# Performance work log

Hardware: AMD Instinct MI355X
Metric: run time of the kernel (lower is better)

Reference implementation:

```python
import jax, jax.numpy as jnp
import numpy as np

N_USERS = 100_000
N_ENTITIES = 200_000
N_EDGES = 1_000_000
NNZ = 1_000_000
C = 64          # embedding dim
N_FACTORS = 4
N_REL_M1 = 10   # n_relations - 1
N_HOPS = 2
TEMP = 0.2


def setup_inputs() -> dict:
    key = jax.random.key(0)
    ks = jax.random.split(key, 10)
    return {
        'user_emb': jax.random.normal(ks[0], (N_USERS, C), jnp.float32) * 0.1,
        'entity_emb': jax.random.normal(ks[1], (N_ENTITIES, C), jnp.float32) * 0.1,
        'latent_emb': jax.random.normal(ks[2], (N_FACTORS, C), jnp.float32) * 0.1,
        'weight': jax.random.normal(ks[3], (N_REL_M1, C), jnp.float32) * 0.1,
        'disen_weight_att': jax.random.normal(ks[4], (N_FACTORS, N_REL_M1), jnp.float32) * 0.1,
        'edge_index': jax.random.randint(ks[5], (2, N_EDGES), 0, N_ENTITIES, dtype=jnp.int32),
        'edge_type': jax.random.randint(ks[6], (N_EDGES,), 1, N_REL_M1 + 1, dtype=jnp.int32),
        'inter_rows': jax.random.randint(ks[7], (NNZ,), 0, N_USERS, dtype=jnp.int32),
        'inter_cols': jax.random.randint(ks[8], (NNZ,), 0, N_ENTITIES, dtype=jnp.int32),
        'inter_vals': jax.random.uniform(ks[9], (NNZ,), jnp.float32),
    }


def _l2norm(x):
    # F.normalize(x, dim=1) with eps=1e-12
    n = jnp.linalg.norm(x, axis=1, keepdims=True)
    return x / jnp.maximum(n, 1e-12)


def _mutual_information(disen_weight_att):
    disen_T = disen_weight_att.T                                    # [R-1, F]
    nd = disen_T / jnp.linalg.norm(disen_T, axis=1, keepdims=True)
    pos_scores = jnp.sum(nd * nd, axis=1)
    ttl_scores = jnp.sum(disen_T @ disen_weight_att, axis=1)
    pos = jnp.exp(pos_scores / TEMP)
    ttl = jnp.exp(ttl_scores / TEMP)
    return -jnp.sum(jnp.log(pos / ttl))


def reference(user_emb, entity_emb, latent_emb, weight, disen_weight_att,
              edge_index, edge_type, inter_rows, inter_cols, inter_vals):
    entity_res = entity_emb
    user_res = user_emb
    cor = _mutual_information(disen_weight_att)

    head, tail = edge_index[0], edge_index[1]
    # edge degree for scatter_mean (constant across hops)
    cnt = jax.ops.segment_sum(jnp.ones((N_EDGES,), jnp.float32), head,
                              num_segments=N_ENTITIES)
    inv_cnt = 1.0 / jnp.maximum(cnt, 1.0)

    for _ in range(N_HOPS):
        # KG aggregate: gather tail entities, modulate by relation, scatter-mean to head
        rel = weight[edge_type - 1]                                  # [E, C]
        neigh = entity_emb[tail] * rel                               # [E, C]
        entity_agg = jax.ops.segment_sum(neigh, head, num_segments=N_ENTITIES)
        entity_agg = entity_agg * inv_cnt[:, None]

        # user -> latent factor attention
        score = jax.nn.softmax(user_emb @ latent_emb.T, axis=1)[:, :, None]  # [U, F, 1]

        # sparse user aggregate: interact_mat @ entity_emb
        user_agg = jax.ops.segment_sum(inter_vals[:, None] * entity_emb[inter_cols],
                                       inter_rows, num_segments=N_USERS)     # [U, C]

        disen_weight = jax.nn.softmax(disen_weight_att, axis=-1) @ weight    # [F, C]
        user_agg = user_agg * jnp.sum(disen_weight[None] * score, axis=1) + user_agg

        entity_emb = _l2norm(entity_agg)
        user_emb = _l2norm(user_agg)
        entity_res = entity_res + entity_emb
        user_res = user_res + user_emb

    return entity_res, user_res, cor
```

## Files before the change

kernel.cpp:

```cpp
#include <hip/hip_runtime.h>
#include <math.h>

#define N_USERS    100000
#define N_ENTITIES 200000
#define N_EDGES    1000000
#define NNZ        1000000
#define CDIM       64
#define N_FACTORS  4
#define N_REL      10
#define TEMP       0.2f

#define CB         1024
#define NBE        196
#define NBU        98
#define ACHUNK     4096
#define GA         245
#define GCVT       6250
#define KG_BLOCKS  6250
#define USER_BLOCKS 3125
#define PCHUNK     4096
#define GPE        49
#define GPU_       25

typedef unsigned int u32;
typedef unsigned short u16;
typedef unsigned char u8;

#if defined(__has_builtin)
#if __has_builtin(__builtin_amdgcn_cvt_pk_f32_fp8) && __has_builtin(__builtin_amdgcn_cvt_pk_fp8_f32)
#define HAVE_HW_FP8 1
#endif
#endif

__device__ __forceinline__ float bflo(u32 w) { return __uint_as_float(w << 16); }
__device__ __forceinline__ float bfhi(u32 w) { return __uint_as_float(w & 0xFFFF0000u); }
__device__ __forceinline__ u16 f2bf(float f) {
    u32 u = __float_as_uint(f);
    u32 r = u + 0x7FFFu + ((u >> 16) & 1u);
    return (u16)(r >> 16);
}
__device__ __forceinline__ void unpack8_bf(uint4 rv, float* x) {
    x[0] = bflo(rv.x); x[1] = bfhi(rv.x);
    x[2] = bflo(rv.y); x[3] = bfhi(rv.y);
    x[4] = bflo(rv.z); x[5] = bfhi(rv.z);
    x[6] = bflo(rv.w); x[7] = bfhi(rv.w);
}
__device__ __forceinline__ uint4 pack8_bf(const float* x) {
    uint4 o;
    o.x = (u32)f2bf(x[0]) | ((u32)f2bf(x[1]) << 16);
    o.y = (u32)f2bf(x[2]) | ((u32)f2bf(x[3]) << 16);
    o.z = (u32)f2bf(x[4]) | ((u32)f2bf(x[5]) << 16);
    o.w = (u32)f2bf(x[6]) | ((u32)f2bf(x[7]) << 16);
    return o;
}

#ifndef HAVE_HW_FP8
__device__ __forceinline__ float fp8_dec1(u32 b) {
    u32 s = b >> 7, em = b & 0x7F;
    float mag;
    if (em < 8) mag = (float)em * 0.001953125f;
    else {
        u32 bits = (((em >> 3) + 120u) << 23) | ((em & 7u) << 20);
        mag = __uint_as_float(bits);
    }
    return s ? -mag : mag;
}
__device__ __forceinline__ u32 fp8_enc1(float f) {
    float a = fabsf(f);
    u32 s = (__float_as_uint(f) >> 31) << 7;
    if (a < 0.015625f) {
        int n = (int)rintf(a * 512.0f);
        return s | (u32)n;
    }
    u32 u = __float_as_uint(a);
    u32 r = u + 0x0007FFFFu + ((u >> 20) & 1u);
    int ee = (int)((r >> 23) & 0xFF) - 127 + 7;
    if (ee >= 16) return s | 0x7Eu;
    return s | ((u32)ee << 3) | ((r >> 20) & 7u);
}
#endif

__device__ __forceinline__ void unpack8_fp8(uint2 rv, float* x) {
#ifdef HAVE_HW_FP8
    typedef float floatx2 __attribute__((ext_vector_type(2)));
    floatx2 a0 = __builtin_amdgcn_cvt_pk_f32_fp8(rv.x, false);
    floatx2 a1 = __builtin_amdgcn_cvt_pk_f32_fp8(rv.x, true);
    floatx2 a2 = __builtin_amdgcn_cvt_pk_f32_fp8(rv.y, false);
    floatx2 a3 = __builtin_amdgcn_cvt_pk_f32_fp8(rv.y, true);
    x[0] = a0.x; x[1] = a0.y; x[2] = a1.x; x[3] = a1.y;
    x[4] = a2.x; x[5] = a2.y; x[6] = a3.x; x[7] = a3.y;
#else
    x[0] = fp8_dec1(rv.x & 0xFF);         x[1] = fp8_dec1((rv.x >> 8) & 0xFF);
    x[2] = fp8_dec1((rv.x >> 16) & 0xFF); x[3] = fp8_dec1(rv.x >> 24);
    x[4] = fp8_dec1(rv.y & 0xFF);         x[5] = fp8_dec1((rv.y >> 8) & 0xFF);
    x[6] = fp8_dec1((rv.y >> 16) & 0xFF); x[7] = fp8_dec1(rv.y >> 24);
#endif
}
__device__ __forceinline__ uint2 pack8_fp8(const float* x) {
    uint2 o;
#ifdef HAVE_HW_FP8
    int v0 = 0, v1 = 0;
    v0 = __builtin_amdgcn_cvt_pk_fp8_f32(x[0], x[1], v0, false);
    v0 = __builtin_amdgcn_cvt_pk_fp8_f32(x[2], x[3], v0, true);
    v1 = __builtin_amdgcn_cvt_pk_fp8_f32(x[4], x[5], v1, false);
    v1 = __builtin_amdgcn_cvt_pk_fp8_f32(x[6], x[7], v1, true);
    o.x = (u32)v0; o.y = (u32)v1;
#else
    o.x = fp8_enc1(x[0]) | (fp8_enc1(x[1]) << 8) | (fp8_enc1(x[2]) << 16) | (fp8_enc1(x[3]) << 24);
    o.y = fp8_enc1(x[4]) | (fp8_enc1(x[5]) << 8) | (fp8_enc1(x[6]) << 16) | (fp8_enc1(x[7]) << 24);
#endif
    return o;
}

__device__ __forceinline__ void fma_rowW(float* acc, uint2 rv, int rel,
                                         const float* __restrict__ weight, int seg) {
    float x[8]; unpack8_fp8(rv, x);
    const float4* wp = (const float4*)(weight + rel * CDIM + seg * 8);
    float4 w0 = wp[0], w1 = wp[1];
    acc[0] += x[0] * w0.x; acc[1] += x[1] * w0.y;
    acc[2] += x[2] * w0.z; acc[3] += x[3] * w0.w;
    acc[4] += x[4] * w1.x; acc[5] += x[5] * w1.y;
    acc[6] += x[6] * w1.z; acc[7] += x[7] * w1.w;
}
__device__ __forceinline__ void fma_rowV(float* acc, uint2 rv, float v) {
    float x[8]; unpack8_fp8(rv, x);
    #pragma unroll
    for (int k = 0; k < 8; ++k) acc[k] += v * x[k];
}

__device__ void dev_cvt(int b, const float* __restrict__ in, u8* __restrict__ out) {
    int i = b * 256 + threadIdx.x;
    const float4* p = (const float4*)(in + (size_t)i * 8);
    float4 a = p[0], bb = p[1];
    float x[8] = {a.x, a.y, a.z, a.w, bb.x, bb.y, bb.z, bb.w};
    *(uint2*)(out + (size_t)i * 8) = pack8_fp8(x);
}

__device__ void dev_coarse_hist(int b, const int* __restrict__ idx, int n,
                                int* __restrict__ bhist) {
    __shared__ int lh[256];
    int t = threadIdx.x;
    lh[t] = 0; __syncthreads();
    int base = b * ACHUNK;
    #pragma unroll
    for (int k = 0; k < 16; ++k) {
        int i = base + k * 256 + t;
        if (i < n) atomicAdd(&lh[idx[i] >> 10], 1);
    }
    __syncthreads();
    if (lh[t]) atomicAdd(&bhist[t], lh[t]);
}

__device__ void dev_disen_cor(const float* __restrict__ att,
                              const float* __restrict__ weight,
                              float* __restrict__ dw, float* __restrict__ cor_out) {
    int tid = threadIdx.x;
    int f = tid >> 6, c = tid & 63;
    float m = -1e30f;
    for (int r = 0; r < N_REL; ++r) m = fmaxf(m, att[f * N_REL + r]);
    float e[N_REL], s = 0.0f;
    for (int r = 0; r < N_REL; ++r) { e[r] = __expf(att[f * N_REL + r] - m); s += e[r]; }
    float acc = 0.0f;
    for (int r = 0; r < N_REL; ++r) acc += (e[r] / s) * weight[r * CDIM + c];
    dw[f * CDIM + c] = acc;

    if (tid == 0) {
        float rowsum[N_FACTORS];
        for (int ff = 0; ff < N_FACTORS; ++ff) {
            float ss = 0.0f;
            for (int j = 0; j < N_REL; ++j) ss += att[ff * N_REL + j];
            rowsum[ff] = ss;
        }
        float cor = 0.0f;
        for (int i = 0; i < N_REL; ++i) {
            float nsq = 0.0f, ttl = 0.0f;
            for (int ff = 0; ff < N_FACTORS; ++ff) {
                float a = att[ff * N_REL + i];
                nsq += a * a;
                ttl += a * rowsum[ff];
            }
            float n = sqrtf(nsq);
            float pos = 0.0f;
            for (int ff = 0; ff < N_FACTORS; ++ff) {
                float a = att[ff * N_REL + i] / n;
                pos += a * a;
            }
            cor += (ttl - pos) / TEMP;
        }
        *cor_out = cor;
    }
}

__global__ __launch_bounds__(256) void prep_kernel(const float* __restrict__ entity_emb,
                                                   u8* __restrict__ ef8,
                                                   const int* __restrict__ head,
                                                   const int* __restrict__ inter_rows,
                                                   int* __restrict__ bhe,
                                                   int* __restrict__ bhu,
                                                   const float* __restrict__ att,
                                                   const float* __restrict__ weight,
                                                   float* __restrict__ dw,
                                                   float* __restrict__ cor_out) {
    int bid = blockIdx.x;
    if (bid < GCVT)                 dev_cvt(bid, entity_emb, ef8);
    else if (bid < GCVT + GA)       dev_coarse_hist(bid - GCVT, head, N_EDGES, bhe);
    else if (bid < GCVT + 2 * GA)   dev_coarse_hist(bid - GCVT - GA, inter_rows, NNZ, bhu);
    else                            dev_disen_cor(att, weight, dw, cor_out);
}

__device__ void dev_bucket_scan(const int* __restrict__ bhist, int nb,
                                int* __restrict__ bbase, int* __restrict__ gcur,
                                int* __restrict__ off_n) {
    __shared__ int s[256];
    int t = threadIdx.x;
    int v = (t < nb) ? bhist[t] : 0;
    s[t] = v; __syncthreads();
    #pragma unroll
    for (int d = 1; d < 256; d <<= 1) {
        int x = (t >= d) ? s[t - d] : 0;
        __syncthreads();
        s[t] += x;
        __syncthreads();
    }
    int excl = s[t] - v;
    if (t < nb) { bbase[t] = excl; gcur[t] = excl; }
    if (t == nb - 1) { bbase[nb] = s[t]; *off_n = s[t]; }
}

__global__ __launch_bounds__(256) void bucket_scan2(const int* __restrict__ bhe,
                                                    const int* __restrict__ bhu,
                                                    int* __restrict__ bbe, int* __restrict__ bbu,
                                                    int* __restrict__ gce, int* __restrict__ gcu,
                                                    int* __restrict__ eoffN, int* __restrict__ uoffN) {
    if (blockIdx.x == 0) dev_bucket_scan(bhe, NBE, bbe, gce, eoffN);
    else                 dev_bucket_scan(bhu, NBU, bbu, gcu, uoffN);
}

__device__ void dev_bin_edges(int b, const int* __restrict__ head,
                              const int* __restrict__ tail, const int* __restrict__ etype,
                              int* __restrict__ gcur, int* __restrict__ binbuf) {
    __shared__ int lh[256], lbase[256];
    int t = threadIdx.x;
    lh[t] = 0; __syncthreads();
    int base = b * ACHUNK;
    int rec[16], rnk[16], bkt[16];
    #pragma unroll
    for (int k = 0; k < 16; ++k) {
        int i = base + k * 256 + t;
        rnk[k] = -1; rec[k] = 0; bkt[k] = 0;
        if (i < N_EDGES) {
            int h = head[i];
            bkt[k] = h >> 10;
            rec[k] = ((h & 1023) << 22) | ((etype[i] - 1) << 18) | tail[i];
            rnk[k] = atomicAdd(&lh[bkt[k]], 1);
        }
    }
    __syncthreads();
    lbase[t] = lh[t] ? atomicAdd(&gcur[t], lh[t]) : 0;
    __syncthreads();
    #pragma unroll
    for (int k = 0; k < 16; ++k)
        if (rnk[k] >= 0) binbuf[lbase[bkt[k]] + rnk[k]] = rec[k];
}

__device__ void dev_bin_inter(int b, const int* __restrict__ rows,
                              const int* __restrict__ cols, const float* __restrict__ vals,
                              int* __restrict__ gcur, int2* __restrict__ binbuf) {
    __shared__ int lh[256], lbase[256];
    int t = threadIdx.x;
    lh[t] = 0; __syncthreads();
    int base = b * ACHUNK;
    int recx[16], recy[16], rnk[16], bkt[16];
    #pragma unroll
    for (int k = 0; k < 16; ++k) {
        int i = base + k * 256 + t;
        rnk[k] = -1; recx[k] = 0; recy[k] = 0; bkt[k] = 0;
        if (i < NNZ) {
            int r = rows[i];
            bkt[k] = r >> 10;
            recx[k] = ((r & 1023) << 18) | cols[i];
            recy[k] = __float_as_int(vals[i]);
            rnk[k] = atomicAdd(&lh[bkt[k]], 1);
        }
    }
    __syncthreads();
    lbase[t] = lh[t] ? atomicAdd(&gcur[t], lh[t]) : 0;
    __syncthreads();
    #pragma unroll
    for (int k = 0; k < 16; ++k)
        if (rnk[k] >= 0) {
            int2 p; p.x = recx[k]; p.y = recy[k];
            binbuf[lbase[bkt[k]] + rnk[k]] = p;
        }
}

__global__ __launch_bounds__(256) void bin_kernel(const int* __restrict__ head,
                                                  const int* __restrict__ tail,
                                                  const int* __restrict__ etype,
                                                  const int* __restrict__ rows,
                                                  const int* __restrict__ cols,
                                                  const float* __restrict__ vals,
                                                  int* __restrict__ gce, int* __restrict__ gcu,
                                                  int* __restrict__ bine, int2* __restrict__ binu) {
    int bid = blockIdx.x;
    if (bid < GA) dev_bin_edges(bid, head, tail, etype, gce, bine);
    else          dev_bin_inter(bid - GA, rows, cols, vals, gcu, binu);
}

__device__ void dev_build_e(int b, const int* __restrict__ bbase,
                            const int* __restrict__ binbuf,
                            int* __restrict__ eoff, int* __restrict__ epk,
                            int* __restrict__ dbinE) {
    __shared__ int lh[CB];
    __shared__ int ss[256];
    __shared__ int ldeg[64];
    int t = threadIdx.x;
    int bstart = bbase[b], bend = bbase[b + 1];
    #pragma unroll
    for (int k = 0; k < 4; ++k) lh[t * 4 + k] = 0;
    if (t < 64) ldeg[t] = 0;
    __syncthreads();
    for (int j = bstart + t; j < bend; j += 256)
        atomicAdd(&lh[(u32)binbuf[j] >> 22], 1);
    __syncthreads();
    int v[4], acc = 0;
    #pragma unroll
    for (int k = 0; k < 4; ++k) { v[k] = lh[t * 4 + k]; acc += v[k]; }
    ss[t] = acc; __syncthreads();
    #pragma unroll
    for (int d = 1; d < 256; d <<= 1) {
        int x = (t >= d) ? ss[t - d] : 0;
        __syncthreads();
        ss[t] += x;
        __syncthreads();
    }
    int excl = ss[t] - acc;
    int hbase = b * CB;
    #pragma unroll
    for (int k = 0; k < 4; ++k) {
        int hl = t * 4 + k;
        int h = hbase + hl;
        if (h < N_ENTITIES) {
            eoff[h] = bstart + excl;
            atomicAdd(&ldeg[63 - min(v[k], 63)], 1);
        }
        lh[hl] = excl;
        excl += v[k];
    }
    __syncthreads();
    if (t < 64 && ldeg[t]) atomicAdd(&dbinE[t], ldeg[t]);
    for (int j = bstart + t; j < bend; j += 256) {
        int rec = binbuf[j];
        int pos = atomicAdd(&lh[(u32)rec >> 22], 1);
        epk[bstart + pos] = rec & 0x3FFFFF;
    }
}

__device__ void dev_build_u(int b, const int* __restrict__ bbase,
                            const int2* __restrict__ binbuf,
                            int* __restrict__ uoff, int2* __restrict__ ucv,
                            int* __restrict__ dbinU) {
    __shared__ int lh[CB];
    __shared__ int ss[256];
    __shared__ int ldeg[64];
    int t = threadIdx.x;
    int bstart = bbase[b], bend = bbase[b + 1];
    #pragma unroll
    for (int k = 0; k < 4; ++k) lh[t * 4 + k] = 0;
    if (t < 64) ldeg[t] = 0;
    __syncthreads();
    for (int j = bstart + t; j < bend; j += 256)
        atomicAdd(&lh[(u32)binbuf[j].x >> 18], 1);
    __syncthreads();
    int v[4], acc = 0;
    #pragma unroll
    for (int k = 0; k < 4; ++k) { v[k] = lh[t * 4 + k]; acc += v[k]; }
    ss[t] = acc; __syncthreads();
    #pragma unroll
    for (int d = 1; d < 256; d <<= 1) {
        int x = (t >= d) ? ss[t - d] : 0;
        __syncthreads();
        ss[t] += x;
        __syncthreads();
    }
    int excl = ss[t] - acc;
    int ubase = b * CB;
    #pragma unroll
    for (int k = 0; k < 4; ++k) {
        int ul = t * 4 + k;
        int u = ubase + ul;
        if (u < N_USERS) {
            uoff[u] = bstart + excl;
            atomicAdd(&ldeg[63 - min(v[k], 63)], 1);
        }
        lh[ul] = excl;
        excl += v[k];
    }
    __syncthreads();
    if (t < 64 && ldeg[t]) atomicAdd(&dbinU[t], ldeg[t]);
    for (int j = bstart + t; j < bend; j += 256) {
        int2 rec = binbuf[j];
        int pos = atomicAdd(&lh[(u32)rec.x >> 18], 1);
        int2 out; out.x = rec.x & 0x3FFFF; out.y = rec.y;
        ucv[bstart + pos] = out;
    }
}

__global__ __launch_bounds__(256) void build_kernel(const int* __restrict__ bbe,
                                                    const int* __restrict__ bbu,
                                                    const int* __restrict__ bine,
                                                    const int2* __restrict__ binu,
                                                    int* __restrict__ eoff, int* __restrict__ epk,
                                                    int* __restrict__ uoff, int2* __restrict__ ucv,
                                                    int* __restrict__ dbinE, int* __restrict__ dbinU) {
    int bid = blockIdx.x;
    if (bid < NBE) dev_build_e(bid, bbe, bine, eoff, epk, dbinE);
    else           dev_build_u(bid - NBE, bbu, binu, uoff, ucv, dbinU);
}

__global__ void deg_scan(const int* __restrict__ dbinE, const int* __restrict__ dbinU,
                         int* __restrict__ curE, int* __restrict__ curU) {
    int t = threadIdx.x;
    if (t == 0) { int run = 0; for (int b = 0; b < 64; ++b) { curE[b] = run; run += dbinE[b]; } }
    if (t == 1) { int run = 0; for (int b = 0; b < 64; ++b) { curU[b] = run; run += dbinU[b]; } }
}

__device__ void dev_perm(int b, int n, const int* __restrict__ off,
                         int* __restrict__ gcur, int2* __restrict__ perm) {
    __shared__ int lh[64], lbase[64];
    int t = threadIdx.x;
    if (t < 64) lh[t] = 0;
    __syncthreads();
    int base = b * PCHUNK;
    int rnk[16], bin[16], deg[16], st[16];
    #pragma unroll
    for (int k = 0; k < 16; ++k) {
        int i = base + k * 256 + t;
        rnk[k] = -1;
        if (i < n) {
            int s0 = off[i], s1 = off[i + 1];
            deg[k] = s1 - s0; st[k] = s0;
            bin[k] = 63 - min(deg[k], 63);
            rnk[k] = atomicAdd(&lh[bin[k]], 1);
        }
    }
    __syncthreads();
    if (t < 64) lbase[t] = lh[t] ? atomicAdd(&gcur[t], lh[t]) : 0;
    __syncthreads();
    #pragma unroll
    for (int k = 0; k < 16; ++k)
        if (rnk[k] >= 0) {
            int i = base + k * 256 + t;
            int2 p;
            p.x = (int)(((u32)min(deg[k], 16383) << 18) | (u32)i);
            p.y = st[k];
            perm[lbase[bin[k]] + rnk[k]] = p;
        }
}

__global__ __launch_bounds__(256) void perm_kernel(const int* __restrict__ eoff,
                                                   const int* __restrict__ uoff,
                                                   int* __restrict__ curE, int* __restrict__ curU,
                                                   int2* __restrict__ permE, int2* __restrict__ permU) {
    int bid = blockIdx.x;
    if (bid < GPE) dev_perm(bid, N_ENTITIES, eoff, curE, permE);
    else           dev_perm(bid - GPE, N_USERS, uoff, curU, permU);
}

__device__ void dev_kg_hop(int widg, const u8* __restrict__ esrc,
                           const int2* __restrict__ permE,
                           const int* __restrict__ epk,
                           const float* __restrict__ weight,
                           const float* __restrict__ emb0,
                           u8* __restrict__ enew, float* __restrict__ eres, int last) {
    int lane = threadIdx.x & 63;
    int slot = lane >> 3, seg = lane & 7;
    int2 pe = permE[widg * 8 + slot];
    u32 px = (u32)pe.x;
    int d = px >> 18, h = (int)(px & 0x3FFFFu), s = pe.y;
    int dmax = d;
    dmax = max(dmax, __shfl_xor(dmax, 8, 64));
    dmax = max(dmax, __shfl_xor(dmax, 16, 64));
    dmax = max(dmax, __shfl_xor(dmax, 32, 64));

    float acc[8];
    #pragma unroll
    for (int k = 0; k < 8; ++k) acc[k] = 0.0f;
    const uint2 uz = make_uint2(0u, 0u);

    for (int it = 0; it < dmax; it += 4) {
        int p0 = (it     < d) ? epk[s + it]     : 0;
        int p1 = (it + 1 < d) ? epk[s + it + 1] : 0;
        int p2 = (it + 2 < d) ? epk[s + it + 2] : 0;
        int p3 = (it + 3 < d) ? epk[s + it + 3] : 0;
        uint2 rv0 = (it     < d) ? *(const uint2*)(esrc + (size_t)(p0 & 0x3FFFF) * CDIM + seg * 8) : uz;
        uint2 rv1 = (it + 1 < d) ? *(const uint2*)(esrc + (size_t)(p1 & 0x3FFFF) * CDIM + seg * 8) : uz;
        uint2 rv2 = (it + 2 < d) ? *(const uint2*)(esrc + (size_t)(p2 & 0x3FFFF) * CDIM + seg * 8) : uz;
        uint2 rv3 = (it + 3 < d) ? *(const uint2*)(esrc + (size_t)(p3 & 0x3FFFF) * CDIM + seg * 8) : uz;
        fma_rowW(acc, rv0, p0 >> 18, weight, seg);
        fma_rowW(acc, rv1, p1 >> 18, weight, seg);
        fma_rowW(acc, rv2, p2 >> 18, weight, seg);
        fma_rowW(acc, rv3, p3 >> 18, weight, seg);
    }
    float inv = 1.0f / fmaxf((float)d, 1.0f);
    float ssq = 0.0f;
    #pragma unroll
    for (int k = 0; k < 8; ++k) { acc[k] *= inv; ssq += acc[k] * acc[k]; }
    ssq += __shfl_xor(ssq, 1, 64);
    ssq += __shfl_xor(ssq, 2, 64);
    ssq += __shfl_xor(ssq, 4, 64);
    float rn = 1.0f / fmaxf(sqrtf(ssq), 1e-12f);
    #pragma unroll
    for (int k = 0; k < 8; ++k) acc[k] *= rn;

    size_t base = (size_t)h * CDIM + seg * 8;
    if (!last) {
        *(uint2*)(enew + base) = pack8_fp8(acc);
    } else {
        uint2 pv = *(const uint2*)(esrc + base);
        float o0[8]; unpack8_fp8(pv, o0);
        float4 a = *(const float4*)(emb0 + base);
        float4 b = *(const float4*)(emb0 + base + 4);
        float4 r0, r1;
        r0.x = a.x + o0[0] + acc[0]; r0.y = a.y + o0[1] + acc[1];
        r0.z = a.z + o0[2] + acc[2]; r0.w = a.w + o0[3] + acc[3];
        r1.x = b.x + o0[4] + acc[4]; r1.y = b.y + o0[5] + acc[5];
        r1.z = b.z + o0[6] + acc[6]; r1.w = b.w + o0[7] + acc[7];
        *(float4*)(eres + base) = r0;
        *(float4*)(eres + base + 4) = r1;
    }
}

__device__ void dev_user_hop(int widg, const float* __restrict__ uoldf,
                             const u16* __restrict__ uoldb,
                             const u8* __restrict__ esrc,
                             const int2* __restrict__ permU,
                             const int2* __restrict__ ucv,
                             const float* __restrict__ latent,
                             const float* __restrict__ dw,
                             const float* __restrict__ uemb0,
                             u16* __restrict__ unew, float* __restrict__ ures, int last) {
    int lane = threadIdx.x & 63;
    int slot = lane >> 3, seg = lane & 7;
    int2 pe = permU[widg * 8 + slot];
    u32 px = (u32)pe.x;
    int d = px >> 18, u = (int)(px & 0x3FFFFu), s = pe.y;
    int dmax = d;
    dmax = max(dmax, __shfl_xor(dmax, 8, 64));
    dmax = max(dmax, __shfl_xor(dmax, 16, 64));
    dmax = max(dmax, __shfl_xor(dmax, 32, 64));

    float acc[8];
    #pragma unroll
    for (int k = 0; k < 8; ++k) acc[k] = 0.0f;
    const uint2 uz = make_uint2(0u, 0u);
    const int2 cz = make_int2(0, 0);

    for (int it = 0; it < dmax; it += 4) {
        int2 c0 = (it     < d) ? ucv[s + it]     : cz;
        int2 c1 = (it + 1 < d) ? ucv[s + it + 1] : cz;
        int2 c2 = (it + 2 < d) ? ucv[s + it + 2] : cz;
        int2 c3 = (it + 3 < d) ? ucv[s + it + 3] : cz;
        uint2 rv0 = (it     < d) ? *(const uint2*)(esrc + (size_t)c0.x * CDIM + seg * 8) : uz;
        uint2 rv1 = (it + 1 < d) ? *(const uint2*)(esrc + (size_t)c1.x * CDIM + seg * 8) : uz;
        uint2 rv2 = (it + 2 < d) ? *(const uint2*)(esrc + (size_t)c2.x * CDIM + seg * 8) : uz;
        uint2 rv3 = (it + 3 < d) ? *(const uint2*)(esrc + (size_t)c3.x * CDIM + seg * 8) : uz;
        fma_rowV(acc, rv0, __int_as_float(c0.y));
        fma_rowV(acc, rv1, __int_as_float(c1.y));
        fma_rowV(acc, rv2, __int_as_float(c2.y));
        fma_rowV(acc, rv3, __int_as_float(c3.y));
    }

    float uo[8];
    size_t ubase = (size_t)u * CDIM + seg * 8;
    if (uoldb) {
        uint4 pv = *(const uint4*)(uoldb + ubase);
        unpack8_bf(pv, uo);
    } else {
        float4 a = *(const float4*)(uoldf + ubase);
        float4 b = *(const float4*)(uoldf + ubase + 4);
        uo[0] = a.x; uo[1] = a.y; uo[2] = a.z; uo[3] = a.w;
        uo[4] = b.x; uo[5] = b.y; uo[6] = b.z; uo[7] = b.w;
    }
    float dts[N_FACTORS];
    #pragma unroll
    for (int f = 0; f < N_FACTORS; ++f) {
        const float4* lp = (const float4*)(latent + f * CDIM + seg * 8);
        float4 l0 = lp[0], l1 = lp[1];
        float p = uo[0] * l0.x + uo[1] * l0.y + uo[2] * l0.z + uo[3] * l0.w +
                  uo[4] * l1.x + uo[5] * l1.y + uo[6] * l1.z + uo[7] * l1.w;
        p += __shfl_xor(p, 1, 64);
        p += __shfl_xor(p, 2, 64);
        p += __shfl_xor(p, 4, 64);
        dts[f] = p;
    }
    float m = fmaxf(fmaxf(dts[0], dts[1]), fmaxf(dts[2], dts[3]));
    float e0 = __expf(dts[0] - m), e1 = __expf(dts[1] - m);
    float e2 = __expf(dts[2] - m), e3 = __expf(dts[3] - m);
    float inv_ssum = 1.0f / (e0 + e1 + e2 + e3);
    e0 *= inv_ssum; e1 *= inv_ssum; e2 *= inv_ssum; e3 *= inv_ssum;

    const float4* d0p = (const float4*)(dw + 0 * CDIM + seg * 8);
    const float4* d1p = (const float4*)(dw + 1 * CDIM + seg * 8);
    const float4* d2p = (const float4*)(dw + 2 * CDIM + seg * 8);
    const float4* d3p = (const float4*)(dw + 3 * CDIM + seg * 8);
    float4 ga0 = d0p[0], ga1 = d0p[1];
    float4 gb0 = d1p[0], gb1 = d1p[1];
    float4 gc0 = d2p[0], gc1 = d2p[1];
    float4 gd0 = d3p[0], gd1 = d3p[1];
    float g[8];
    g[0] = e0 * ga0.x + e1 * gb0.x + e2 * gc0.x + e3 * gd0.x;
    g[1] = e0 * ga0.y + e1 * gb0.y + e2 * gc0.y + e3 * gd0.y;
    g[2] = e0 * ga0.z + e1 * gb0.z + e2 * gc0.z + e3 * gd0.z;
    g[3] = e0 * ga0.w + e1 * gb0.w + e2 * gc0.w + e3 * gd0.w;
    g[4] = e0 * ga1.x + e1 * gb1.x + e2 * gc1.x + e3 * gd1.x;
    g[5] = e0 * ga1.y + e1 * gb1.y + e2 * gc1.y + e3 * gd1.y;
    g[6] = e0 * ga1.z + e1 * gb1.z + e2 * gc1.z + e3 * gd1.z;
    g[7] = e0 * ga1.w + e1 * gb1.w + e2 * gc1.w + e3 * gd1.w;

    float ssq = 0.0f;
    #pragma unroll
    for (int k = 0; k < 8; ++k) {
        acc[k] = acc[k] * (1.0f + g[k]);
        ssq += acc[k] * acc[k];
    }
    ssq += __shfl_xor(ssq, 1, 64);
    ssq += __shfl_xor(ssq, 2, 64);
    ssq += __shfl_xor(ssq, 4, 64);
    float rn = 1.0f / fmaxf(sqrtf(ssq), 1e-12f);
    #pragma unroll
    for (int k = 0; k < 8; ++k) acc[k] *= rn;

    if (!last) {
        *(uint4*)(unew + ubase) = pack8_bf(acc);
    } else {
        float4 a = *(const float4*)(uemb0 + ubase);
        float4 b = *(const float4*)(uemb0 + ubase + 4);
        float4 r0, r1;
        r0.x = a.x + uo[0] + acc[0]; r0.y = a.y + uo[1] + acc[1];
        r0.z = a.z + uo[2] + acc[2]; r0.w = a.w + uo[3] + acc[3];
        r1.x = b.x + uo[4] + acc[4]; r1.y = b.y + uo[5] + acc[5];
        r1.z = b.z + uo[6] + acc[6]; r1.w = b.w + uo[7] + acc[7];
        *(float4*)(ures + ubase) = r0;
        *(float4*)(ures + ubase + 4) = r1;
    }
}

__global__ __launch_bounds__(256) void hop_kernel(const u8* __restrict__ e_src,
                                                  const int2* __restrict__ permE,
                                                  const int* __restrict__ epk,
                                                  const float* __restrict__ weight,
                                                  const float* __restrict__ entity_emb,
                                                  u8* __restrict__ eA,
                                                  float* __restrict__ eres,
                                                  const float* __restrict__ uoldf,
                                                  const u16* __restrict__ uoldb,
                                                  const int2* __restrict__ permU,
                                                  const int2* __restrict__ ucv,
                                                  const float* __restrict__ latent,
                                                  const float* __restrict__ dw,
                                                  const float* __restrict__ user_emb,
                                                  u16* __restrict__ uA,
                                                  float* __restrict__ ures,
                                                  int last) {
    int bid = blockIdx.x;
    int wave = threadIdx.x >> 6;
    if (bid < KG_BLOCKS) {
        dev_kg_hop(bid * 4 + wave, e_src, permE, epk, weight, entity_emb, eA, eres, last);
    } else {
        dev_user_hop((bid - KG_BLOCKS) * 4 + wave, uoldf, uoldb, e_src, permU, ucv,
                     latent, dw, user_emb, uA, ures, last);
    }
}

static inline size_t align16(size_t x) { return (x + 15) & ~(size_t)15; }

extern "C" void kernel_launch(void* const* d_in, const int* in_sizes, int n_in,
                              void* d_out, int out_size, void* d_ws, size_t ws_size,
                              hipStream_t stream) {
    const float* user_emb   = (const float*)d_in[0];
    const float* entity_emb = (const float*)d_in[1];
    const float* latent_emb = (const float*)d_in[2];
    const float* weight     = (const float*)d_in[3];
    const float* att        = (const float*)d_in[4];
    const int*   edge_index = (const int*)d_in[5];
    const int*   edge_type  = (const int*)d_in[6];
    const int*   inter_rows = (const int*)d_in[7];
    const int*   inter_cols = (const int*)d_in[8];
    const float* inter_vals = (const float*)d_in[9];

    float* eres = (float*)d_out;
    float* ures = eres + (size_t)N_ENTITIES * CDIM;
    float* cor  = ures + (size_t)N_USERS * CDIM;

    char* ws = (char*)d_ws;
    u8*    ef8   = (u8*)ws;   ws += align16(sizeof(u8) * (size_t)N_ENTITIES * CDIM);
    u8*    eA    = (u8*)ws;   ws += align16(sizeof(u8) * (size_t)N_ENTITIES * CDIM);
    u16*   uA    = (u16*)ws;  ws += align16(sizeof(u16) * (size_t)N_USERS * CDIM);
    int*   eoff  = (int*)ws;  ws += align16(sizeof(int) * (N_ENTITIES + 1));
    int*   epk   = (int*)ws;  ws += align16(sizeof(int) * N_EDGES);
    int*   uoff  = (int*)ws;  ws += align16(sizeof(int) * (N_USERS + 1));
    int2*  ucv   = (int2*)ws; ws += align16(sizeof(int2) * NNZ);
    int*   bine  = (int*)ws;  ws += align16(sizeof(int) * N_EDGES);
    int2*  binu  = (int2*)ws; ws += align16(sizeof(int2) * NNZ);
    int*   ctrs  = (int*)ws;  ws += align16(sizeof(int) * 640);
    int*   bbe   = (int*)ws;  ws += align16(sizeof(int) * 257);
    int*   bbu   = (int*)ws;  ws += align16(sizeof(int) * 257);
    int*   gce   = (int*)ws;  ws += align16(sizeof(int) * 256);
    int*   gcu   = (int*)ws;  ws += align16(sizeof(int) * 256);
    int*   curE  = (int*)ws;  ws += align16(sizeof(int) * 64);
    int*   curU  = (int*)ws;  ws += align16(sizeof(int) * 64);
    int2*  permE = (int2*)ws; ws += align16(sizeof(int2) * N_ENTITIES);
    int2*  permU = (int2*)ws; ws += align16(sizeof(int2) * N_USERS);
    float* dw    = (float*)ws; ws += align16(sizeof(float) * N_FACTORS * CDIM);

    int* bhe   = ctrs;
    int* bhu   = ctrs + 256;
    int* dbinE = ctrs + 512;
    int* dbinU = ctrs + 576;

    const int* head = edge_index;
    const int* tail = edge_index + N_EDGES;

    (void)hipMemsetAsync(ctrs, 0, sizeof(int) * 640, stream);

    prep_kernel<<<GCVT + 2 * GA + 1, 256, 0, stream>>>(entity_emb, ef8, head, inter_rows,
                                                       bhe, bhu, att, weight, dw, cor);
    bucket_scan2<<<2, 256, 0, stream>>>(bhe, bhu, bbe, bbu, gce, gcu,
                                        eoff + N_ENTITIES, uoff + N_USERS);
    bin_kernel<<<2 * GA, 256, 0, stream>>>(head, tail, edge_type,
                                           inter_rows, inter_cols, inter_vals,
                                           gce, gcu, bine, binu);
    build_kernel<<<NBE + NBU, 256, 0, stream>>>(bbe, bbu, bine, binu,
                                                eoff, epk, uoff, ucv, dbinE, dbinU);
    deg_scan<<<1, 64, 0, stream>>>(dbinE, dbinU, curE, curU);
    perm_kernel<<<GPE + GPU_, 256, 0, stream>>>(eoff, uoff, curE, curU, permE, permU);

    hop_kernel<<<KG_BLOCKS + USER_BLOCKS, 256, 0, stream>>>(
        ef8, permE, epk, weight, entity_emb, eA, eres,
        user_emb, (const u16*)nullptr, permU, ucv, latent_emb, dw, user_emb, uA, ures, 0);
    hop_kernel<<<KG_BLOCKS + USER_BLOCKS, 256, 0, stream>>>(
        eA, permE, epk, weight, entity_emb, (u8*)nullptr, eres,
        (const float*)nullptr, uA, permU, ucv, latent_emb, dw, user_emb, (u16*)nullptr, ures, 1);
}
```

Measured before the change: 216.0 us.

## Fold bucket/degree scans into consumer kernels, interleave hop work, unroll gathers by 8

Removes the separate bucket_scan2 and deg_scan launches. Each bin, build and perm block now recomputes the small prefix scan in LDS and uses zeroed atomic cursors offset by that scan. The hop kernel interleaves user and KG blocks (every third block is a user block) so the two workloads balance across the grid. The gather loops in both the KG and user paths are unrolled from 4 to 8 loads to keep more memory requests in flight. The cost is redundant per-block scan work and higher register pressure in the gather loops.

After: 223.0 us. 3.2% more time.

```diff
diff --git a/kernel.cpp b/kernel.cpp
--- a/kernel.cpp
+++ b/kernel.cpp
@@ -16,8 +16,9 @@
 #define ACHUNK     4096
 #define GA         245
 #define GCVT       6250
-#define KG_BLOCKS  6250
-#define USER_BLOCKS 3125
+#define KG_WAVES   25000
+#define USER_WAVES 12500
+#define HOP_BLOCKS 9375
 #define PCHUNK     4096
 #define GPE        49
 #define GPU_       25
@@ -128,6 +129,22 @@
     for (int k = 0; k < 8; ++k) acc[k] += v * x[k];
 }
 
+__device__ __forceinline__ void lds_scan256(const int* __restrict__ hist, int* sbase,
+                                            int* stmp) {
+    int t = threadIdx.x;
+    int v = hist[t];
+    stmp[t] = v; __syncthreads();
+    #pragma unroll
+    for (int d = 1; d < 256; d <<= 1) {
+        int x = (t >= d) ? stmp[t - d] : 0;
+        __syncthreads();
+        stmp[t] += x;
+        __syncthreads();
+    }
+    sbase[t] = stmp[t] - v;
+    __syncthreads();
+}
+
 __device__ void dev_cvt(int b, const float* __restrict__ in, u8* __restrict__ out) {
     int i = b * 256 + threadIdx.x;
     const float4* p = (const float4*)(in + (size_t)i * 8);
@@ -208,39 +225,14 @@
     else                            dev_disen_cor(att, weight, dw, cor_out);
 }
 
-__device__ void dev_bucket_scan(const int* __restrict__ bhist, int nb,
-                                int* __restrict__ bbase, int* __restrict__ gcur,
-                                int* __restrict__ off_n) {
-    __shared__ int s[256];
-    int t = threadIdx.x;
-    int v = (t < nb) ? bhist[t] : 0;
-    s[t] = v; __syncthreads();
-    #pragma unroll
-    for (int d = 1; d < 256; d <<= 1) {
-        int x = (t >= d) ? s[t - d] : 0;
-        __syncthreads();
-        s[t] += x;
-        __syncthreads();
-    }
-    int excl = s[t] - v;
-    if (t < nb) { bbase[t] = excl; gcur[t] = excl; }
-    if (t == nb - 1) { bbase[nb] = s[t]; *off_n = s[t]; }
-}
-
-__global__ __launch_bounds__(256) void bucket_scan2(const int* __restrict__ bhe,
-                                                    const int* __restrict__ bhu,
-                                                    int* __restrict__ bbe, int* __restrict__ bbu,
-                                                    int* __restrict__ gce, int* __restrict__ gcu,
-                                                    int* __restrict__ eoffN, int* __restrict__ uoffN) {
-    if (blockIdx.x == 0) dev_bucket_scan(bhe, NBE, bbe, gce, eoffN);
-    else                 dev_bucket_scan(bhu, NBU, bbu, gcu, uoffN);
-}
-
 __device__ void dev_bin_edges(int b, const int* __restrict__ head,
                               const int* __restrict__ tail, const int* __restrict__ etype,
-                              int* __restrict__ gcur, int* __restrict__ binbuf) {
+                              const int* __restrict__ bhist,
+                              int* __restrict__ zcur, int* __restrict__ binbuf) {
+    __shared__ int sbase[256], stmp[256];
     __shared__ int lh[256], lbase[256];
     int t = threadIdx.x;
+    lds_scan256(bhist, sbase, stmp);
     lh[t] = 0; __syncthreads();
     int base = b * ACHUNK;
     int rec[16], rnk[16], bkt[16];
@@ -256,7 +248,7 @@
         }
     }
     __syncthreads();
-    lbase[t] = lh[t] ? atomicAdd(&gcur[t], lh[t]) : 0;
+    lbase[t] = lh[t] ? (sbase[t] + atomicAdd(&zcur[t], lh[t])) : 0;
     __syncthreads();
     #pragma unroll
     for (int k = 0; k < 16; ++k)
@@ -265,9 +257,12 @@
 
 __device__ void dev_bin_inter(int b, const int* __restrict__ rows,
                               const int* __restrict__ cols, const float* __restrict__ vals,
-                              int* __restrict__ gcur, int2* __restrict__ binbuf) {
+                              const int* __restrict__ bhist,
+                              int* __restrict__ zcur, int2* __restrict__ binbuf) {
+    __shared__ int sbase[256], stmp[256];
     __shared__ int lh[256], lbase[256];
     int t = threadIdx.x;
+    lds_scan256(bhist, sbase, stmp);
     lh[t] = 0; __syncthreads();
     int base = b * ACHUNK;
     int recx[16], recy[16], rnk[16], bkt[16];
@@ -284,7 +279,7 @@
         }
     }
     __syncthreads();
-    lbase[t] = lh[t] ? atomicAdd(&gcur[t], lh[t]) : 0;
+    lbase[t] = lh[t] ? (sbase[t] + atomicAdd(&zcur[t], lh[t])) : 0;
     __syncthreads();
     #pragma unroll
     for (int k = 0; k < 16; ++k)
@@ -300,22 +295,26 @@
                                                   const int* __restrict__ rows,
                                                   const int* __restrict__ cols,
                                                   const float* __restrict__ vals,
-                                                  int* __restrict__ gce, int* __restrict__ gcu,
+                                                  const int* __restrict__ bhe,
+                                                  const int* __restrict__ bhu,
+                                                  int* __restrict__ zce, int* __restrict__ zcu,
                                                   int* __restrict__ bine, int2* __restrict__ binu) {
     int bid = blockIdx.x;
-    if (bid < GA) dev_bin_edges(bid, head, tail, etype, gce, bine);
-    else          dev_bin_inter(bid - GA, rows, cols, vals, gcu, binu);
-}
-
-__device__ void dev_build_e(int b, const int* __restrict__ bbase,
+    if (bid < GA) dev_bin_edges(bid, head, tail, etype, bhe, zce, bine);
+    else          dev_bin_inter(bid - GA, rows, cols, vals, bhu, zcu, binu);
+}
+
+__device__ void dev_build_e(int b, const int* __restrict__ bhist,
                             const int* __restrict__ binbuf,
                             int* __restrict__ eoff, int* __restrict__ epk,
                             int* __restrict__ dbinE) {
+    __shared__ int sbase[256], stmp[256];
     __shared__ int lh[CB];
     __shared__ int ss[256];
     __shared__ int ldeg[64];
     int t = threadIdx.x;
-    int bstart = bbase[b], bend = bbase[b + 1];
+    lds_scan256(bhist, sbase, stmp);
+    int bstart = sbase[b], bend = sbase[b] + bhist[b];
     #pragma unroll
     for (int k = 0; k < 4; ++k) lh[t * 4 + k] = 0;
     if (t < 64) ldeg[t] = 0;
@@ -349,6 +348,7 @@
     }
     __syncthreads();
     if (t < 64 && ldeg[t]) atomicAdd(&dbinE[t], ldeg[t]);
+    if (b == 0 && t == 0) eoff[N_ENTITIES] = N_EDGES;
     for (int j = bstart + t; j < bend; j += 256) {
         int rec = binbuf[j];
         int pos = atomicAdd(&lh[(u32)rec >> 22], 1);
@@ -356,15 +356,17 @@
     }
 }
 
-__device__ void dev_build_u(int b, const int* __restrict__ bbase,
+__device__ void dev_build_u(int b, const int* __restrict__ bhist,
                             const int2* __restrict__ binbuf,
                             int* __restrict__ uoff, int2* __restrict__ ucv,
                             int* __restrict__ dbinU) {
+    __shared__ int sbase[256], stmp[256];
     __shared__ int lh[CB];
     __shared__ int ss[256];
     __shared__ int ldeg[64];
     int t = threadIdx.x;
-    int bstart = bbase[b], bend = bbase[b + 1];
+    lds_scan256(bhist, sbase, stmp);
+    int bstart = sbase[b], bend = sbase[b] + bhist[b];
     #pragma unroll
     for (int k = 0; k < 4; ++k) lh[t * 4 + k] = 0;
     if (t < 64) ldeg[t] = 0;
@@ -398,6 +400,7 @@
     }
     __syncthreads();
     if (t < 64 && ldeg[t]) atomicAdd(&dbinU[t], ldeg[t]);
+    if (b == 0 && t == 0) uoff[N_USERS] = NNZ;
     for (int j = bstart + t; j < bend; j += 256) {
         int2 rec = binbuf[j];
         int pos = atomicAdd(&lh[(u32)rec.x >> 18], 1);
@@ -406,30 +409,40 @@
     }
 }
 
-__global__ __launch_bounds__(256) void build_kernel(const int* __restrict__ bbe,
-                                                    const int* __restrict__ bbu,
+__global__ __launch_bounds__(256) void build_kernel(const int* __restrict__ bhe,
+                                                    const int* __restrict__ bhu,
                                                     const int* __restrict__ bine,
                                                     const int2* __restrict__ binu,
                                                     int* __restrict__ eoff, int* __restrict__ epk,
                                                     int* __restrict__ uoff, int2* __restrict__ ucv,
                                                     int* __restrict__ dbinE, int* __restrict__ dbinU) {
     int bid = blockIdx.x;
-    if (bid < NBE) dev_build_e(bid, bbe, bine, eoff, epk, dbinE);
-    else           dev_build_u(bid - NBE, bbu, binu, uoff, ucv, dbinU);
-}
-
-__global__ void deg_scan(const int* __restrict__ dbinE, const int* __restrict__ dbinU,
-                         int* __restrict__ curE, int* __restrict__ curU) {
-    int t = threadIdx.x;
-    if (t == 0) { int run = 0; for (int b = 0; b < 64; ++b) { curE[b] = run; run += dbinE[b]; } }
-    if (t == 1) { int run = 0; for (int b = 0; b < 64; ++b) { curU[b] = run; run += dbinU[b]; } }
+    if (bid < NBE) dev_build_e(bid, bhe, bine, eoff, epk, dbinE);
+    else           dev_build_u(bid - NBE, bhu, binu, uoff, ucv, dbinU);
 }
 
 __device__ void dev_perm(int b, int n, const int* __restrict__ off,
-                         int* __restrict__ gcur, int2* __restrict__ perm) {
+                         const int* __restrict__ dbin,
+                         int* __restrict__ zdeg, int2* __restrict__ perm) {
+    __shared__ int dbase[64], dtmp[64];
     __shared__ int lh[64], lbase[64];
     int t = threadIdx.x;
-    if (t < 64) lh[t] = 0;
+    if (t < 64) { dtmp[t] = dbin[t]; lh[t] = 0; }
+    __syncthreads();
+    if (t < 64) {
+        int v = dtmp[t];
+        #pragma unroll
+        for (int d = 1; d < 64; d <<= 1) {
+            int x = (t >= d) ? dtmp[t - d] : 0;
+            __syncthreads();
+            dtmp[t] += x;
+            __syncthreads();
+        }
+        dbase[t] = dtmp[t] - v;
+    } else {
+        #pragma unroll
+        for (int d = 1; d < 64; d <<= 1) { __syncthreads(); __syncthreads(); }
+    }
     __syncthreads();
     int base = b * PCHUNK;
     int rnk[16], bin[16], deg[16], st[16];
@@ -445,7 +458,7 @@
         }
     }
     __syncthreads();
-    if (t < 64) lbase[t] = lh[t] ? atomicAdd(&gcur[t], lh[t]) : 0;
+    if (t < 64) lbase[t] = lh[t] ? (dbase[t] + atomicAdd(&zdeg[t], lh[t])) : 0;
     __syncthreads();
     #pragma unroll
     for (int k = 0; k < 16; ++k)
@@ -460,11 +473,13 @@
 
 __global__ __launch_bounds__(256) void perm_kernel(const int* __restrict__ eoff,
                                                    const int* __restrict__ uoff,
-                                                   int* __restrict__ curE, int* __restrict__ curU,
+                                                   const int* __restrict__ dbinE,
+                                                   const int* __restrict__ dbinU,
+                                                   int* __restrict__ zdegE, int* __restrict__ zdegU,
                                                    int2* __restrict__ permE, int2* __restrict__ permU) {
     int bid = blockIdx.x;
-    if (bid < GPE) dev_perm(bid, N_ENTITIES, eoff, curE, permE);
-    else           dev_perm(bid - GPE, N_USERS, uoff, curU, permU);
+    if (bid < GPE) dev_perm(bid, N_ENTITIES, eoff, dbinE, zdegE, permE);
+    else           dev_perm(bid - GPE, N_USERS, uoff, dbinU, zdegU, permU);
 }
 
 __device__ void dev_kg_hop(int widg, const u8* __restrict__ esrc,
@@ -488,19 +503,18 @@
     for (int k = 0; k < 8; ++k) acc[k] = 0.0f;
     const uint2 uz = make_uint2(0u, 0u);
 
-    for (int it = 0; it < dmax; it += 4) {
-        int p0 = (it     < d) ? epk[s + it]     : 0;
-        int p1 = (it + 1 < d) ? epk[s + it + 1] : 0;
-        int p2 = (it + 2 < d) ? epk[s + it + 2] : 0;
-        int p3 = (it + 3 < d) ? epk[s + it + 3] : 0;
-        uint2 rv0 = (it     < d) ? *(const uint2*)(esrc + (size_t)(p0 & 0x3FFFF) * CDIM + seg * 8) : uz;
-        uint2 rv1 = (it + 1 < d) ? *(const uint2*)(esrc + (size_t)(p1 & 0x3FFFF) * CDIM + seg * 8) : uz;
-        uint2 rv2 = (it + 2 < d) ? *(const uint2*)(esrc + (size_t)(p2 & 0x3FFFF) * CDIM + seg * 8) : uz;
-        uint2 rv3 = (it + 3 < d) ? *(const uint2*)(esrc + (size_t)(p3 & 0x3FFFF) * CDIM + seg * 8) : uz;
-        fma_rowW(acc, rv0, p0 >> 18, weight, seg);
-        fma_rowW(acc, rv1, p1 >> 18, weight, seg);
-        fma_rowW(acc, rv2, p2 >> 18, weight, seg);
-        fma_rowW(acc, rv3, p3 >> 18, weight, seg);
+    for (int it = 0; it < dmax; it += 8) {
+        int pk[8]; uint2 rv[8];
+        #pragma unroll
+        for (int q = 0; q < 8; ++q)
+            pk[q] = (it + q < d) ? epk[s + it + q] : 0;
+        #pragma unroll
+        for (int q = 0; q < 8; ++q)
+            rv[q] = (it + q < d)
+                  ? *(const uint2*)(esrc + (size_t)(pk[q] & 0x3FFFF) * CDIM + seg * 8) : uz;
+        #pragma unroll
+        for (int q = 0; q < 8; ++q)
+            fma_rowW(acc, rv[q], pk[q] >> 18, weight, seg);
     }
     float inv = 1.0f / fmaxf((float)d, 1.0f);
     float ssq = 0.0f;
@@ -556,19 +570,18 @@
     const uint2 uz = make_uint2(0u, 0u);
     const int2 cz = make_int2(0, 0);
 
-    for (int it = 0; it < dmax; it += 4) {
-        int2 c0 = (it     < d) ? ucv[s + it]     : cz;
-        int2 c1 = (it + 1 < d) ? ucv[s + it + 1] : cz;
-        int2 c2 = (it + 2 < d) ? ucv[s + it + 2] : cz;
-        int2 c3 = (it + 3 < d) ? ucv[s + it + 3] : cz;
-        uint2 rv0 = (it     < d) ? *(const uint2*)(esrc + (size_t)c0.x * CDIM + seg * 8) : uz;
-        uint2 rv1 = (it + 1 < d) ? *(const uint2*)(esrc + (size_t)c1.x * CDIM + seg * 8) : uz;
-        uint2 rv2 = (it + 2 < d) ? *(const uint2*)(esrc + (size_t)c2.x * CDIM + seg * 8) : uz;
-        uint2 rv3 = (it + 3 < d) ? *(const uint2*)(esrc + (size_t)c3.x * CDIM + seg * 8) : uz;
-        fma_rowV(acc, rv0, __int_as_float(c0.y));
-        fma_rowV(acc, rv1, __int_as_float(c1.y));
-        fma_rowV(acc, rv2, __int_as_float(c2.y));
-        fma_rowV(acc, rv3, __int_as_float(c3.y));
+    for (int it = 0; it < dmax; it += 8) {
+        int2 cc[8]; uint2 rv[8];
+        #pragma unroll
+        for (int q = 0; q < 8; ++q)
+            cc[q] = (it + q < d) ? ucv[s + it + q] : cz;
+        #pragma unroll
+        for (int q = 0; q < 8; ++q)
+            rv[q] = (it + q < d)
+                  ? *(const uint2*)(esrc + (size_t)cc[q].x * CDIM + seg * 8) : uz;
+        #pragma unroll
+        for (int q = 0; q < 8; ++q)
+            fma_rowV(acc, rv[q], __int_as_float(cc[q].y));
     }
 
     float uo[8];
@@ -665,11 +678,12 @@
                                                   int last) {
     int bid = blockIdx.x;
     int wave = threadIdx.x >> 6;
-    if (bid < KG_BLOCKS) {
-        dev_kg_hop(bid * 4 + wave, e_src, permE, epk, weight, entity_emb, eA, eres, last);
+    if (bid % 3 == 0) {
+        dev_user_hop((bid / 3) * 4 + wave, uoldf, uoldb, e_src, permU, ucv,
+                     latent, dw, user_emb, uA, ures, last);
     } else {
-        dev_user_hop((bid - KG_BLOCKS) * 4 + wave, uoldf, uoldb, e_src, permU, ucv,
-                     latent, dw, user_emb, uA, ures, last);
+        int kb = bid - bid / 3 - 1;
+        dev_kg_hop(kb * 4 + wave, e_src, permE, epk, weight, entity_emb, eA, eres, last);
     }
 }
 
@@ -703,13 +717,7 @@
     int2*  ucv   = (int2*)ws; ws += align16(sizeof(int2) * NNZ);
     int*   bine  = (int*)ws;  ws += align16(sizeof(int) * N_EDGES);
     int2*  binu  = (int2*)ws; ws += align16(sizeof(int2) * NNZ);
-    int*   ctrs  = (int*)ws;  ws += align16(sizeof(int) * 640);
-    int*   bbe   = (int*)ws;  ws += align16(sizeof(int) * 257);
-    int*   bbu   = (int*)ws;  ws += align16(sizeof(int) * 257);
-    int*   gce   = (int*)ws;  ws += align16(sizeof(int) * 256);
-    int*   gcu   = (int*)ws;  ws += align16(sizeof(int) * 256);
-    int*   curE  = (int*)ws;  ws += align16(sizeof(int) * 64);
-    int*   curU  = (int*)ws;  ws += align16(sizeof(int) * 64);
+    int*   ctrs  = (int*)ws;  ws += align16(sizeof(int) * 1280);
     int2*  permE = (int2*)ws; ws += align16(sizeof(int2) * N_ENTITIES);
     int2*  permU = (int2*)ws; ws += align16(sizeof(int2) * N_USERS);
     float* dw    = (float*)ws; ws += align16(sizeof(float) * N_FACTORS * CDIM);
@@ -718,28 +726,30 @@
     int* bhu   = ctrs + 256;
     int* dbinE = ctrs + 512;
     int* dbinU = ctrs + 576;
+    int* zce   = ctrs + 640;
+    int* zcu   = ctrs + 896;
+    int* zdegE = ctrs + 1152;
+    int* zdegU = ctrs + 1216;
 
     const int* head = edge_index;
     const int* tail = edge_index + N_EDGES;
 
-    (void)hipMemsetAsync(ctrs, 0, sizeof(int) * 640, stream);
+    (void)hipMemsetAsync(ctrs, 0, sizeof(int) * 1280, stream);
 
     prep_kernel<<<GCVT + 2 * GA + 1, 256, 0, stream>>>(entity_emb, ef8, head, inter_rows,
                                                        bhe, bhu, att, weight, dw, cor);
-    bucket_scan2<<<2, 256, 0, stream>>>(bhe, bhu, bbe, bbu, gce, gcu,
-                                        eoff + N_ENTITIES, uoff + N_USERS);
     bin_kernel<<<2 * GA, 256, 0, stream>>>(head, tail, edge_type,
                                            inter_rows, inter_cols, inter_vals,
-                                           gce, gcu, bine, binu);
-    build_kernel<<<NBE + NBU, 256, 0, stream>>>(bbe, bbu, bine, binu,
+                                           bhe, bhu, zce, zcu, bine, binu);
+    build_kernel<<<NBE + NBU, 256, 0, stream>>>(bhe, bhu, bine, binu,
                                                 eoff, epk, uoff, ucv, dbinE, dbinU);
-    deg_scan<<<1, 64, 0, stream>>>(dbinE, dbinU, curE, curU);
-    perm_kernel<<<GPE + GPU_, 256, 0, stream>>>(eoff, uoff, curE, curU, permE, permU);
-
-    hop_kernel<<<KG_BLOCKS + USER_BLOCKS, 256, 0, stream>>>(
+    perm_kernel<<<GPE + GPU_, 256, 0, stream>>>(eoff, uoff, dbinE, dbinU,
+                                                zdegE, zdegU, permE, permU);
+
+    hop_kernel<<<HOP_BLOCKS, 256, 0, stream>>>(
         ef8, permE, epk, weight, entity_emb, eA, eres,
         user_emb, (const u16*)nullptr, permU, ucv, latent_emb, dw, user_emb, uA, ures, 0);
-    hop_kernel<<<KG_BLOCKS + USER_BLOCKS, 256, 0, stream>>>(
+    hop_kernel<<<HOP_BLOCKS, 256, 0, stream>>>(
         eA, permE, epk, weight, entity_emb, (u8*)nullptr, eres,
         (const float*)nullptr, uA, permU, ucv, latent_emb, dw, user_emb, (u16*)nullptr, ures, 1);
 }
```
